# Optimization experiments

Hardware: AMD Instinct MI355X
Metric: run time of the kernel (lower is better)

The kernel has to match this reference:

```python
import jax, jax.numpy as jnp
import numpy as np

N = 50000; E = 800000; IN = 256; HID = 128; H = 4; C = 32; L = 3
REL = 100; RD = 16; EH = 32  # rel_emb_dim, edge-encoder hidden
LN_EPS = 1e-5


def _ln(x, g, b):
    m = jnp.mean(x, axis=-1, keepdims=True)
    v = jnp.mean((x - m) ** 2, axis=-1, keepdims=True)
    return (x - m) * jax.lax.rsqrt(v + LN_EPS) * g + b


def _mlp2(x, W1, b1, W2, b2):
    return jax.nn.relu(x @ W1 + b1) @ W2 + b2


def _forward(x, edge_attr, in_g, in_b, proj_W, proj_b,
             dist_W1, dist_b1, dist_W2, dist_b2,
             coexp_W1, coexp_b1, coexp_W2, coexp_b2,
             rel_emb, fus_W1, fus_b1, fus_ln_g, fus_ln_b, fus_W2, fus_b2,
             Wsrc, Wdst, Wedge, att, sscale, ng, nb, edge_index):
    src, dst = edge_index[0], edge_index[1]
    dist_w = edge_attr[:, 0]                              # [E] raw distance weight
    # ---- edge encoder ----
    dist_feat = _mlp2(edge_attr[:, 0:1], dist_W1, dist_b1, dist_W2, dist_b2)   # [E,RD]
    coexp_feat = _mlp2(edge_attr[:, 1:2], coexp_W1, coexp_b1, coexp_W2, coexp_b2)
    rel_id = jnp.clip(edge_attr[:, 2].astype(jnp.int32), 0, REL - 1)
    rel_feat = rel_emb[rel_id]                            # [E,RD]
    comb = jnp.concatenate([dist_feat, coexp_feat, rel_feat], axis=1)          # [E,3*RD]
    h = comb @ fus_W1 + fus_b1
    h = jax.nn.relu(_ln(h, fus_ln_g, fus_ln_b))
    edge_feat = h @ fus_W2 + fus_b2                       # [E,RD]
    # ---- input norm + projection ----
    x = _ln(x, in_g, in_b) @ proj_W + proj_b              # [N,HID]
    # ---- GAT layers ----
    for i in range(L):
        x_res = x
        xs = (x @ Wsrc[i]).reshape(N, H, C)
        xd = (x @ Wdst[i]).reshape(N, H, C)
        ef = (edge_feat @ Wedge[i]).reshape(E, H, C)
        a = jnp.tanh(xs[src] + xd[dst] + ef)              # [E,H,C]
        alpha = jnp.sum(a * att[i][None], axis=-1)        # [E,H]
        if i < L - 1:  # spatial_decay on all but last layer
            alpha = alpha * (dist_w[:, None] ** sscale[i][None, :])
        amax = jax.ops.segment_max(alpha, dst, num_segments=N)   # [N,H]
        ea = jnp.exp(alpha - amax[dst])
        esum = jax.ops.segment_sum(ea, dst, num_segments=N)
        alpha = ea / (esum[dst] + 1e-8)                   # [E,H]
        msg = xs[src] * alpha[..., None]                  # [E,H,C]
        out = jax.ops.segment_sum(msg, dst, num_segments=N).reshape(N, H * C)
        x = jax.nn.elu(_ln(out, ng[i], nb[i])) + x_res
    return x


def setup_inputs() -> dict:
    key = jax.random.key(0)
    ks = jax.random.split(key, 24)
    p = lambda k, s: jax.random.normal(k, s, jnp.float32) * 0.05
    edge_attr = jnp.concatenate([
        jax.random.uniform(ks[2], (E, 2), jnp.float32, 0.01, 1.0),
        jax.random.randint(ks[3], (E, 1), 0, REL).astype(jnp.float32)], axis=1)
    return dict(
        x=jax.random.normal(ks[0], (N, IN), jnp.float32),
        edge_index=jax.random.randint(ks[1], (2, E), 0, N),
        edge_attr=edge_attr,
        in_g=jnp.ones((IN,), jnp.float32), in_b=jnp.zeros((IN,), jnp.float32),
        proj_W=p(ks[4], (IN, HID)), proj_b=jnp.zeros((HID,), jnp.float32),
        dist_W1=p(ks[5], (1, EH)), dist_b1=jnp.zeros((EH,), jnp.float32),
        dist_W2=p(ks[6], (EH, RD)), dist_b2=jnp.zeros((RD,), jnp.float32),
        coexp_W1=p(ks[7], (1, EH)), coexp_b1=jnp.zeros((EH,), jnp.float32),
        coexp_W2=p(ks[8], (EH, RD)), coexp_b2=jnp.zeros((RD,), jnp.float32),
        rel_emb=p(ks[9], (REL, RD)),
        fus_W1=p(ks[10], (3 * RD, 2 * RD)), fus_b1=jnp.zeros((2 * RD,), jnp.float32),
        fus_ln_g=jnp.ones((2 * RD,), jnp.float32), fus_ln_b=jnp.zeros((2 * RD,), jnp.float32),
        fus_W2=p(ks[11], (2 * RD, RD)), fus_b2=jnp.zeros((RD,), jnp.float32),
        Wsrc=p(ks[12], (L, HID, HID)), Wdst=p(ks[13], (L, HID, HID)),
        Wedge=p(ks[14], (L, RD, HID)), att=p(ks[15], (L, H, C)),
        sscale=jnp.ones((L, H), jnp.float32),
        ng=jnp.ones((L, HID), jnp.float32), nb=jnp.zeros((L, HID), jnp.float32),
    )


def reference(x, edge_index, edge_attr, in_g, in_b, proj_W, proj_b,
              dist_W1, dist_b1, dist_W2, dist_b2,
              coexp_W1, coexp_b1, coexp_W2, coexp_b2,
              rel_emb, fus_W1, fus_b1, fus_ln_g, fus_ln_b, fus_W2, fus_b2,
              Wsrc, Wdst, Wedge, att, sscale, ng, nb):
    return _forward(x, edge_attr, in_g, in_b, proj_W, proj_b,
                    dist_W1, dist_b1, dist_W2, dist_b2,
                    coexp_W1, coexp_b1, coexp_W2, coexp_b2,
                    rel_emb, fus_W1, fus_b1, fus_ln_g, fus_ln_b, fus_W2, fus_b2,
                    Wsrc, Wdst, Wedge, att, sscale, ng, nb, edge_index)
```

## Files before the change

kernel.cpp:

```cpp
#include <hip/hip_runtime.h>
#include <math.h>

#define NN 50000
#define NE 800000
#define IND 256
#define HD 128
#define NH 4
#define NC 32
#define RELN 100
#define RD 16
#define EHD 32

typedef unsigned int uint;
typedef _Float16 half2_t __attribute__((ext_vector_type(2)));

__device__ inline uint pack_bf16(float a, float b) {
    uint ua = __float_as_uint(a), ub = __float_as_uint(b);
    ua += 0x7fffu + ((ua >> 16) & 1u);
    ub += 0x7fffu + ((ub >> 16) & 1u);
    return (ua >> 16) | (ub & 0xffff0000u);
}

__device__ inline uint pack_f16(float a, float b) {
    half2_t h = { (_Float16)a, (_Float16)b };
    return __builtin_bit_cast(uint, h);
}

#if __has_builtin(__builtin_amdgcn_fdot2)
#define FDOT2(a, b, c) __builtin_amdgcn_fdot2((a), (b), (c), false)
#else
static __device__ inline float FDOT2(half2_t a, half2_t b, float c) {
    return c + (float)a.x * (float)b.x + (float)a.y * (float)b.y;
}
#endif

__global__ __launch_bounds__(256) void count_kernel(
    const int* __restrict__ dst, int* __restrict__ counts)
{
    int e = blockIdx.x * 256 + threadIdx.x;
    if (e < NE) atomicAdd(&counts[dst[e]], 1);
}

__global__ __launch_bounds__(1024) void scan_kernel(
    const int* __restrict__ counts, int* __restrict__ row_ptr,
    int* __restrict__ cursor, int n)
{
    __shared__ int wsum[16];
    int tid = threadIdx.x;
    int C = (n + 1023) >> 10;
    int lo = tid * C, hi = min(lo + C, n);
    int s = 0;
    for (int i = lo; i < hi; i++) s += counts[i];
    int lane = tid & 63;
    int incl = s;
#pragma unroll
    for (int off = 1; off < 64; off <<= 1) {
        int v = __shfl_up(incl, off);
        if (lane >= off) incl += v;
    }
    if (lane == 63) wsum[tid >> 6] = incl;
    __syncthreads();
    if (tid < 16) {
        int v = wsum[tid];
        int inc2 = v;
#pragma unroll
        for (int off = 1; off < 16; off <<= 1) {
            int u = __shfl_up(inc2, off);
            if (tid >= off) inc2 += u;
        }
        wsum[tid] = inc2 - v;
    }
    __syncthreads();
    int run = wsum[tid >> 6] + (incl - s);
    for (int i = lo; i < hi; i++) {
        row_ptr[i] = run; cursor[i] = run; run += counts[i];
    }
    if (tid == 1023) row_ptr[n] = run;
}

__global__ __launch_bounds__(256) void edge_feat_fill_kernel(
    const float* __restrict__ eattr, const int* __restrict__ src,
    const int* __restrict__ dst, int* __restrict__ cursor,
    const float* __restrict__ dW1, const float* __restrict__ db1,
    const float* __restrict__ dW2, const float* __restrict__ db2,
    const float* __restrict__ cW1, const float* __restrict__ cb1,
    const float* __restrict__ cW2, const float* __restrict__ cb2,
    const float* __restrict__ rel_emb,
    const float* __restrict__ fW1, const float* __restrict__ fb1,
    const float* __restrict__ fg,  const float* __restrict__ fbl,
    const float* __restrict__ fW2, const float* __restrict__ fb2,
    uint4* __restrict__ efeat_h, int2* __restrict__ meta_c)
{
    int e = blockIdx.x * 256 + threadIdx.x;
    if (e >= NE) return;
    float d  = eattr[(size_t)e * 3 + 0];
    float cx = eattr[(size_t)e * 3 + 1];
    int r = (int)eattr[(size_t)e * 3 + 2];
    r = min(max(r, 0), RELN - 1);
    int p = atomicAdd(&cursor[dst[e]], 1);
    meta_c[p] = make_int2(src[e], __float_as_int(__log2f(d)));

    float df[RD], cf[RD];
#pragma unroll
    for (int k = 0; k < RD; k++) { df[k] = db2[k]; cf[k] = cb2[k]; }
    for (int j = 0; j < EHD; j++) {
        float h1 = fmaxf(d  * dW1[j] + db1[j], 0.f);
        float h2 = fmaxf(cx * cW1[j] + cb1[j], 0.f);
#pragma unroll
        for (int k = 0; k < RD; k++) {
            df[k] += h1 * dW2[j * RD + k];
            cf[k] += h2 * cW2[j * RD + k];
        }
    }
    float hh[2 * RD];
#pragma unroll
    for (int m = 0; m < 2 * RD; m++) hh[m] = fb1[m];
    for (int k = 0; k < RD; k++) {
        float a = df[k], b = cf[k], c = rel_emb[r * RD + k];
#pragma unroll
        for (int m = 0; m < 2 * RD; m++) {
            hh[m] += a * fW1[k * (2 * RD) + m]
                   + b * fW1[(RD + k) * (2 * RD) + m]
                   + c * fW1[(2 * RD + k) * (2 * RD) + m];
        }
    }
    float s = 0.f;
#pragma unroll
    for (int m = 0; m < 2 * RD; m++) s += hh[m];
    float mean = s * (1.f / (2 * RD));
    float s2 = 0.f;
#pragma unroll
    for (int m = 0; m < 2 * RD; m++) { float dd = hh[m] - mean; s2 += dd * dd; }
    float rs = rsqrtf(s2 * (1.f / (2 * RD)) + 1e-5f);
#pragma unroll
    for (int m = 0; m < 2 * RD; m++)
        hh[m] = fmaxf((hh[m] - mean) * rs * fg[m] + fbl[m], 0.f);

    float ef[RD];
#pragma unroll
    for (int k = 0; k < RD; k++) ef[k] = fb2[k];
    for (int m = 0; m < 2 * RD; m++) {
        float hv = hh[m];
#pragma unroll
        for (int k = 0; k < RD; k++) ef[k] += hv * fW2[m * RD + k];
    }
    uint4 e0, e1;
    e0.x = pack_f16(ef[0],  ef[1]);  e0.y = pack_f16(ef[2],  ef[3]);
    e0.z = pack_f16(ef[4],  ef[5]);  e0.w = pack_f16(ef[6],  ef[7]);
    e1.x = pack_f16(ef[8],  ef[9]);  e1.y = pack_f16(ef[10], ef[11]);
    e1.z = pack_f16(ef[12], ef[13]); e1.w = pack_f16(ef[14], ef[15]);
    efeat_h[(size_t)p * 2 + 0] = e0;
    efeat_h[(size_t)p * 2 + 1] = e1;
}

__global__ __launch_bounds__(256) void ln_proj_kernel(
    const float* __restrict__ x, const float* __restrict__ g, const float* __restrict__ b,
    const float* __restrict__ W, const float* __restrict__ pb, float* __restrict__ x0)
{
    __shared__ float xr[8][IND];
    __shared__ float mv[8][2];
    int nb = blockIdx.x * 8;
    int tid = threadIdx.x;
    const float4* xv = (const float4*)(x + (size_t)nb * IND);
    float4* xl = (float4*)&xr[0][0];
    xl[tid] = xv[tid];
    xl[tid + 256] = xv[tid + 256];
    __syncthreads();
    int node = tid >> 5, lane = tid & 31;
    float s1 = 0.f, s2 = 0.f;
#pragma unroll
    for (int j = 0; j < 8; j++) { float v = xr[node][lane + 32 * j]; s1 += v; s2 += v * v; }
#pragma unroll
    for (int off = 16; off >= 1; off >>= 1) { s1 += __shfl_xor(s1, off); s2 += __shfl_xor(s2, off); }
    if (lane == 0) {
        float mean = s1 * (1.f / IND);
        mv[node][0] = mean;
        mv[node][1] = rsqrtf(s2 * (1.f / IND) - mean * mean + 1e-5f);
    }
    __syncthreads();
#pragma unroll
    for (int j = 0; j < 8; j++) {
        int k = lane + 32 * j;
        xr[node][k] = (xr[node][k] - mv[node][0]) * mv[node][1] * g[k] + b[k];
    }
    __syncthreads();
    int col = tid & 127, r0 = (tid >> 7) * 4;
    float acc[4] = {0.f, 0.f, 0.f, 0.f};
    for (int k = 0; k < IND; k += 4) {
        float4 x4[4];
#pragma unroll
        for (int r = 0; r < 4; r++) x4[r] = *(const float4*)&xr[r0 + r][k];
        float w0 = W[(k + 0) * HD + col];
        float w1 = W[(k + 1) * HD + col];
        float w2 = W[(k + 2) * HD + col];
        float w3 = W[(k + 3) * HD + col];
#pragma unroll
        for (int r = 0; r < 4; r++)
            acc[r] += x4[r].x * w0 + x4[r].y * w1 + x4[r].z * w2 + x4[r].w * w3;
    }
    float pbv = pb[col];
#pragma unroll
    for (int r = 0; r < 4; r++)
        x0[(size_t)(nb + r0 + r) * HD + col] = acc[r] + pbv;
}

__global__ __launch_bounds__(256) void gemm_sd_kernel(
    const float* __restrict__ x, const float* __restrict__ Ws, const float* __restrict__ Wd,
    uint* __restrict__ xs_p, float2* __restrict__ xd2)
{
    __shared__ float xt[32][HD];
    int nb = blockIdx.x * 32;
    int tid = threadIdx.x;
    const float4* xv = (const float4*)(x + (size_t)nb * HD);
    float4* xl = (float4*)&xt[0][0];
    int validf4 = (NN - nb >= 32) ? 1024 : (NN - nb) * 32;
    for (int idx = tid; idx < 1024; idx += 256) {
        float4 v = {0.f, 0.f, 0.f, 0.f};
        if (idx < validf4) v = xv[idx];
        xl[idx] = v;
    }
    __syncthreads();
    int cp = tid & 63;
    int r0 = (tid >> 6) * 8;
#pragma unroll
    for (int ct = 0; ct < 2; ct++) {
        const float2* W2v = (const float2*)(ct ? Wd : Ws);
        float a0[8] = {0.f}, a1[8] = {0.f};
        for (int k = 0; k < HD; k += 4) {
            float4 x4[8];
#pragma unroll
            for (int r = 0; r < 8; r++) x4[r] = *(const float4*)&xt[r0 + r][k];
            float2 w0 = W2v[(k + 0) * 64 + cp];
            float2 w1 = W2v[(k + 1) * 64 + cp];
            float2 w2 = W2v[(k + 2) * 64 + cp];
            float2 w3 = W2v[(k + 3) * 64 + cp];
#pragma unroll
            for (int r = 0; r < 8; r++) {
                a0[r] += x4[r].x * w0.x + x4[r].y * w1.x + x4[r].z * w2.x + x4[r].w * w3.x;
                a1[r] += x4[r].x * w0.y + x4[r].y * w1.y + x4[r].z * w2.y + x4[r].w * w3.y;
            }
        }
        if (ct == 0) {
#pragma unroll
            for (int r = 0; r < 8; r++) {
                int n = nb + r0 + r;
                if (n < NN) xs_p[(size_t)n * 64 + cp] = pack_bf16(a0[r], a1[r]);
            }
        } else {
#pragma unroll
            for (int r = 0; r < 8; r++) {
                int n = nb + r0 + r;
                if (n < NN) xd2[(size_t)n * 64 + cp] = make_float2(a0[r], a1[r]);
            }
        }
    }
}

__global__ __launch_bounds__(256) void aggregate_kernel(
    const uint* __restrict__ xs_p, const float2* __restrict__ xd2,
    const uint4* __restrict__ efeat_h, const int2* __restrict__ meta_c,
    const int* __restrict__ row_ptr,
    const float* __restrict__ Wedge_i, const float2* __restrict__ att2,
    const float* __restrict__ sscale_i, const float2* __restrict__ ng2,
    const float2* __restrict__ nb2, float2* __restrict__ xio2,
    int apply_dist, int nwaves)
{
    int l = threadIdx.x & 63;
    int wid = blockIdx.x * 4 + __builtin_amdgcn_readfirstlane(threadIdx.x >> 6);

    int c0 = 2 * l, c1 = 2 * l + 1;
    half2_t wxh[8], wyh[8];
#pragma unroll
    for (int q = 0; q < 8; q++) {
        wxh[q] = (half2_t){ (_Float16)Wedge_i[(2 * q) * HD + c0],
                            (_Float16)Wedge_i[(2 * q + 1) * HD + c0] };
        wyh[q] = (half2_t){ (_Float16)Wedge_i[(2 * q) * HD + c1],
                            (_Float16)Wedge_i[(2 * q + 1) * HD + c1] };
    }
    float2 attv = att2[l];
    float sc = sscale_i[l >> 4];
    float2 g = ng2[l], bb = nb2[l];

    for (int node = wid; node < NN; node += nwaves) {
        int e0 = row_ptr[node], e1 = row_ptr[node + 1];
        float2 xdv  = xd2[(size_t)node * 64 + l];
        float2 xres = xio2[(size_t)node * 64 + l];
        float esum = 0.f;
        float2 macc = {0.f, 0.f};

        if (e0 < e1) {
            int2 mt[4]; uint xw[4]; uint4 ef[4][2];
#pragma unroll
            for (int j = 0; j < 4; j++) {
                int pp = min(e0 + j, e1 - 1);
                mt[j] = meta_c[pp];
                ef[j][0] = efeat_h[(size_t)pp * 2 + 0];
                ef[j][1] = efeat_h[(size_t)pp * 2 + 1];
            }
#pragma unroll
            for (int j = 0; j < 4; j++) xw[j] = xs_p[(size_t)mt[j].x * 64 + l];

#pragma unroll 2
            for (int b = e0; b < e1; b += 4) {
                int bn = b + 4;
                bool more = bn < e1;
                int2 mtn[4]; uint xwn[4]; uint4 efn[4][2];
                if (more) {
#pragma unroll
                    for (int j = 0; j < 4; j++) {
                        int pp = min(bn + j, e1 - 1);
                        mtn[j] = meta_c[pp];
                        efn[j][0] = efeat_h[(size_t)pp * 2 + 0];
                        efn[j][1] = efeat_h[(size_t)pp * 2 + 1];
                    }
#pragma unroll
                    for (int j = 0; j < 4; j++) xwn[j] = xs_p[(size_t)mtn[j].x * 64 + l];
                }
#pragma unroll
                for (int j = 0; j < 4; j++) {
                    const half2_t* eh = (const half2_t*)&ef[j][0];
                    float efx = 0.f, efy = 0.f;
#pragma unroll
                    for (int q = 0; q < 8; q++) {
                        efx = FDOT2(eh[q], wxh[q], efx);
                        efy = FDOT2(eh[q], wyh[q], efy);
                    }
                    float xvx = __uint_as_float(xw[j] << 16);
                    float xvy = __uint_as_float(xw[j] & 0xffff0000u);
                    float zx = xvx + xdv.x + efx;
                    float zy = xvy + xdv.y + efy;
                    float tx = 1.f - 2.f * __builtin_amdgcn_rcpf(__expf(2.f * zx) + 1.f);
                    float ty = 1.f - 2.f * __builtin_amdgcn_rcpf(__expf(2.f * zy) + 1.f);
                    float a = tx * attv.x + ty * attv.y;
#pragma unroll
                    for (int off = 8; off >= 1; off >>= 1) a += __shfl_xor(a, off);
                    if (apply_dist) a *= exp2f(__int_as_float(mt[j].y) * sc);
                    float ea = __expf(a);
                    ea = (b + j < e1) ? ea : 0.f;
                    esum += ea;
                    macc.x += xvx * ea;
                    macc.y += xvy * ea;
                }
                if (more) {
#pragma unroll
                    for (int j = 0; j < 4; j++) {
                        mt[j] = mtn[j]; xw[j] = xwn[j];
                        ef[j][0] = efn[j][0]; ef[j][1] = efn[j][1];
                    }
                }
            }
        }
        float inv = __builtin_amdgcn_rcpf(esum + 1e-8f);
        float2 outv = { macc.x * inv, macc.y * inv };

        float s1 = outv.x + outv.y;
        float s2 = outv.x * outv.x + outv.y * outv.y;
#pragma unroll
        for (int off = 32; off >= 1; off >>= 1) { s1 += __shfl_xor(s1, off); s2 += __shfl_xor(s2, off); }
        float mean = s1 * (1.f / HD);
        float var = s2 * (1.f / HD) - mean * mean;
        float rstd = rsqrtf(var + 1e-5f);
        float yx = (outv.x - mean) * rstd * g.x + bb.x;
        float yy = (outv.y - mean) * rstd * g.y + bb.y;
        float ex = (yx > 0.f) ? yx : expm1f(yx);
        float ey = (yy > 0.f) ? yy : expm1f(yy);
        float2 res;
        res.x = ex + xres.x;
        res.y = ey + xres.y;
        xio2[(size_t)node * 64 + l] = res;
    }
}

extern "C" void kernel_launch(void* const* d_in, const int* in_sizes, int n_in,
                              void* d_out, int out_size, void* d_ws, size_t ws_size,
                              hipStream_t stream)
{
    const float* x_in   = (const float*)d_in[0];
    const int*   eidx   = (const int*)  d_in[1];
    const float* eattr  = (const float*)d_in[2];
    const float* in_g   = (const float*)d_in[3];
    const float* in_b   = (const float*)d_in[4];
    const float* proj_W = (const float*)d_in[5];
    const float* proj_b = (const float*)d_in[6];
    const float* dW1    = (const float*)d_in[7];
    const float* db1    = (const float*)d_in[8];
    const float* dW2    = (const float*)d_in[9];
    const float* db2    = (const float*)d_in[10];
    const float* cW1    = (const float*)d_in[11];
    const float* cb1    = (const float*)d_in[12];
    const float* cW2    = (const float*)d_in[13];
    const float* cb2    = (const float*)d_in[14];
    const float* rel_emb= (const float*)d_in[15];
    const float* fW1    = (const float*)d_in[16];
    const float* fb1    = (const float*)d_in[17];
    const float* fg     = (const float*)d_in[18];
    const float* fbl    = (const float*)d_in[19];
    const float* fW2    = (const float*)d_in[20];
    const float* fb2    = (const float*)d_in[21];
    const float* Wsrc   = (const float*)d_in[22];
    const float* Wdst   = (const float*)d_in[23];
    const float* Wedge  = (const float*)d_in[24];
    const float* att    = (const float*)d_in[25];
    const float* sscale = (const float*)d_in[26];
    const float* ng     = (const float*)d_in[27];
    const float* nb     = (const float*)d_in[28];

    const int* src = eidx;
    const int* dst = eidx + NE;

    char* p = (char*)d_ws;
    auto alloc = [&](size_t bytes) -> void* {
        void* r = p;
        p += (bytes + 255) & ~(size_t)255;
        return r;
    };
    uint*  xs_p    = (uint*) alloc((size_t)NN * 64 * 4);
    float* xd      = (float*)alloc((size_t)NN * HD * 4);
    uint4* efeat_h = (uint4*)alloc((size_t)NE * 32);
    int*   counts  = (int*)  alloc((size_t)NN * 4);
    int*   row_ptr = (int*)  alloc(((size_t)NN + 1) * 4);
    int*   cursor  = (int*)  alloc((size_t)NN * 4);
    int2*  meta_c  = (int2*) alloc((size_t)NE * 8);

    float* x_cur = (float*)d_out;

    hipMemsetAsync(counts, 0, (size_t)NN * 4, stream);
    hipLaunchKernelGGL(count_kernel, dim3(NE / 256), dim3(256), 0, stream, dst, counts);
    hipLaunchKernelGGL(scan_kernel, dim3(1), dim3(1024), 0, stream,
        counts, row_ptr, cursor, NN);
    hipLaunchKernelGGL(edge_feat_fill_kernel, dim3(NE / 256), dim3(256), 0, stream,
        eattr, src, dst, cursor, dW1, db1, dW2, db2, cW1, cb1, cW2, cb2, rel_emb,
        fW1, fb1, fg, fbl, fW2, fb2, efeat_h, meta_c);
    hipLaunchKernelGGL(ln_proj_kernel, dim3(NN / 8), dim3(256), 0, stream,
        x_in, in_g, in_b, proj_W, proj_b, x_cur);

    const int AGG_BLOCKS = 2048;
    const int NWAVES = AGG_BLOCKS * 4;
    for (int i = 0; i < 3; i++) {
        hipLaunchKernelGGL(gemm_sd_kernel, dim3((NN + 31) / 32), dim3(256), 0, stream,
            x_cur, Wsrc + (size_t)i * HD * HD, Wdst + (size_t)i * HD * HD,
            xs_p, (float2*)xd);
        hipLaunchKernelGGL(aggregate_kernel, dim3(AGG_BLOCKS), dim3(256), 0, stream,
            xs_p, (const float2*)xd, efeat_h, meta_c, row_ptr,
            Wedge + (size_t)i * RD * HD, (const float2*)(att + (size_t)i * NH * NC),
            sscale + (size_t)i * NH,
            (const float2*)(ng + (size_t)i * HD), (const float2*)(nb + (size_t)i * HD),
            (float2*)x_cur, (i < 2) ? 1 : 0, NWAVES);
    }
}
```

Measured before the change: 933.9 us.

## Process two destination nodes per wave with interleaved edge pipelines

Each wave now handles a pair of adjacent destination nodes and interleaves their edge batches, each with its own double-buffered prefetch. The aim is to raise memory-level parallelism for the gathers and hide latency at node boundaries, since a single node's edge list is short. In exchange, register use roughly doubles, which may reduce occupancy. Nodes with unequal degrees also leave one stream idle while the other finishes.

```diff
diff --git a/kernel.cpp b/kernel.cpp
--- a/kernel.cpp
+++ b/kernel.cpp
@@ -281,78 +281,51 @@
     float sc = sscale_i[l >> 4];
     float2 g = ng2[l], bb = nb2[l];
 
-    for (int node = wid; node < NN; node += nwaves) {
-        int e0 = row_ptr[node], e1 = row_ptr[node + 1];
-        float2 xdv  = xd2[(size_t)node * 64 + l];
-        float2 xres = xio2[(size_t)node * 64 + l];
-        float esum = 0.f;
-        float2 macc = {0.f, 0.f};
-
-        if (e0 < e1) {
-            int2 mt[4]; uint xw[4]; uint4 ef[4][2];
-#pragma unroll
-            for (int j = 0; j < 4; j++) {
-                int pp = min(e0 + j, e1 - 1);
-                mt[j] = meta_c[pp];
-                ef[j][0] = efeat_h[(size_t)pp * 2 + 0];
-                ef[j][1] = efeat_h[(size_t)pp * 2 + 1];
-            }
-#pragma unroll
-            for (int j = 0; j < 4; j++) xw[j] = xs_p[(size_t)mt[j].x * 64 + l];
-
-#pragma unroll 2
-            for (int b = e0; b < e1; b += 4) {
-                int bn = b + 4;
-                bool more = bn < e1;
-                int2 mtn[4]; uint xwn[4]; uint4 efn[4][2];
-                if (more) {
-#pragma unroll
-                    for (int j = 0; j < 4; j++) {
-                        int pp = min(bn + j, e1 - 1);
-                        mtn[j] = meta_c[pp];
-                        efn[j][0] = efeat_h[(size_t)pp * 2 + 0];
-                        efn[j][1] = efeat_h[(size_t)pp * 2 + 1];
-                    }
-#pragma unroll
-                    for (int j = 0; j < 4; j++) xwn[j] = xs_p[(size_t)mtn[j].x * 64 + l];
-                }
-#pragma unroll
-                for (int j = 0; j < 4; j++) {
-                    const half2_t* eh = (const half2_t*)&ef[j][0];
-                    float efx = 0.f, efy = 0.f;
-#pragma unroll
-                    for (int q = 0; q < 8; q++) {
-                        efx = FDOT2(eh[q], wxh[q], efx);
-                        efy = FDOT2(eh[q], wyh[q], efy);
-                    }
-                    float xvx = __uint_as_float(xw[j] << 16);
-                    float xvy = __uint_as_float(xw[j] & 0xffff0000u);
-                    float zx = xvx + xdv.x + efx;
-                    float zy = xvy + xdv.y + efy;
-                    float tx = 1.f - 2.f * __builtin_amdgcn_rcpf(__expf(2.f * zx) + 1.f);
-                    float ty = 1.f - 2.f * __builtin_amdgcn_rcpf(__expf(2.f * zy) + 1.f);
-                    float a = tx * attv.x + ty * attv.y;
-#pragma unroll
-                    for (int off = 8; off >= 1; off >>= 1) a += __shfl_xor(a, off);
-                    if (apply_dist) a *= exp2f(__int_as_float(mt[j].y) * sc);
-                    float ea = __expf(a);
-                    ea = (b + j < e1) ? ea : 0.f;
-                    esum += ea;
-                    macc.x += xvx * ea;
-                    macc.y += xvy * ea;
-                }
-                if (more) {
-#pragma unroll
-                    for (int j = 0; j < 4; j++) {
-                        mt[j] = mtn[j]; xw[j] = xwn[j];
-                        ef[j][0] = efn[j][0]; ef[j][1] = efn[j][1];
-                    }
-                }
-            }
-        }
+    auto loadB = [&](int b, int e1, int2* mt, uint* xw, uint4 (*ef)[2]) {
+#pragma unroll
+        for (int j = 0; j < 4; j++) {
+            int pp = min(b + j, e1 - 1);
+            mt[j] = meta_c[pp];
+            ef[j][0] = efeat_h[(size_t)pp * 2 + 0];
+            ef[j][1] = efeat_h[(size_t)pp * 2 + 1];
+        }
+#pragma unroll
+        for (int j = 0; j < 4; j++) xw[j] = xs_p[(size_t)mt[j].x * 64 + l];
+    };
+
+    auto computeB = [&](int b, int e1, const int2* mt, const uint* xw,
+                        const uint4 (*ef)[2], float2 xdv,
+                        float& esum, float2& macc) {
+#pragma unroll
+        for (int j = 0; j < 4; j++) {
+            const half2_t* eh = (const half2_t*)&ef[j][0];
+            float efx = 0.f, efy = 0.f;
+#pragma unroll
+            for (int q = 0; q < 8; q++) {
+                efx = FDOT2(eh[q], wxh[q], efx);
+                efy = FDOT2(eh[q], wyh[q], efy);
+            }
+            float xvx = __uint_as_float(xw[j] << 16);
+            float xvy = __uint_as_float(xw[j] & 0xffff0000u);
+            float zx = xvx + xdv.x + efx;
+            float zy = xvy + xdv.y + efy;
+            float tx = 1.f - 2.f * __builtin_amdgcn_rcpf(__expf(2.f * zx) + 1.f);
+            float ty = 1.f - 2.f * __builtin_amdgcn_rcpf(__expf(2.f * zy) + 1.f);
+            float a = tx * attv.x + ty * attv.y;
+#pragma unroll
+            for (int off = 8; off >= 1; off >>= 1) a += __shfl_xor(a, off);
+            if (apply_dist) a *= exp2f(__int_as_float(mt[j].y) * sc);
+            float ea = __expf(a);
+            ea = (b + j < e1) ? ea : 0.f;
+            esum += ea;
+            macc.x += xvx * ea;
+            macc.y += xvy * ea;
+        }
+    };
+
+    auto epilogue = [&](int node, float esum, float2 macc, float2 xres) {
         float inv = __builtin_amdgcn_rcpf(esum + 1e-8f);
         float2 outv = { macc.x * inv, macc.y * inv };
-
         float s1 = outv.x + outv.y;
         float s2 = outv.x * outv.x + outv.y * outv.y;
 #pragma unroll
@@ -368,6 +341,50 @@
         res.x = ex + xres.x;
         res.y = ey + xres.y;
         xio2[(size_t)node * 64 + l] = res;
+    };
+
+    const int npairs = NN / 2;
+    for (int pr = wid; pr < npairs; pr += nwaves) {
+        int nA = 2 * pr, nB = 2 * pr + 1;
+        int e0A = row_ptr[nA], e1A = row_ptr[nA + 1], e1B = row_ptr[nB + 1];
+        int e0B = e1A;
+        float2 xdvA  = xd2[(size_t)nA * 64 + l], xdvB  = xd2[(size_t)nB * 64 + l];
+        float2 xresA = xio2[(size_t)nA * 64 + l], xresB = xio2[(size_t)nB * 64 + l];
+        float esumA = 0.f, esumB = 0.f;
+        float2 maccA = {0.f, 0.f}, maccB = {0.f, 0.f};
+
+        int2 mtA[4], mtB[4], mtA2[4], mtB2[4];
+        uint xwA[4], xwB[4], xwA2[4], xwB2[4];
+        uint4 efA[4][2], efB[4][2], efA2[4][2], efB2[4][2];
+        int bA = e0A, bB = e0B;
+        if (bA < e1A) loadB(bA, e1A, mtA, xwA, efA);
+        if (bB < e1B) loadB(bB, e1B, mtB, xwB, efB);
+
+        while (bA < e1A || bB < e1B) {
+            bool moreA = (bA + 4) < e1A;
+            bool moreB = (bB + 4) < e1B;
+            if (moreA) loadB(bA + 4, e1A, mtA2, xwA2, efA2);
+            if (moreB) loadB(bB + 4, e1B, mtB2, xwB2, efB2);
+            if (bA < e1A) computeB(bA, e1A, mtA, xwA, efA, xdvA, esumA, maccA);
+            if (bB < e1B) computeB(bB, e1B, mtB, xwB, efB, xdvB, esumB, maccB);
+            if (moreA) {
+#pragma unroll
+                for (int j = 0; j < 4; j++) {
+                    mtA[j] = mtA2[j]; xwA[j] = xwA2[j];
+                    efA[j][0] = efA2[j][0]; efA[j][1] = efA2[j][1];
+                }
+            }
+            if (moreB) {
+#pragma unroll
+                for (int j = 0; j < 4; j++) {
+                    mtB[j] = mtB2[j]; xwB[j] = xwB2[j];
+                    efB[j][0] = efB2[j][0]; efB[j][1] = efB2[j][1];
+                }
+            }
+            bA += 4; bB += 4;
+        }
+        epilogue(nA, esumA, maccA, xresA);
+        epilogue(nB, esumB, maccB, xresB);
     }
 }
 
```

Result: slower. 1.069 ms (+14.5%).
